# Kernel tuning notes

Hardware: AMD Instinct MI355X
Metric: run time of the kernel (lower is better)

Reference implementation:

```python
import jax, jax.numpy as jnp
import numpy as np

N = 50000          # nodes per side (variables == clauses here)
IN, HID, OUT = 64, 128, 128
H = 4              # attention heads (self and cross)
P = 2              # num_meta_paths
E = 640000         # edges per graph
NEG = 0.2          # leaky_relu negative slope


def _glorot(key, shape):
    fan = shape[-2] + shape[-1]
    return (jax.random.normal(key, shape) * jnp.sqrt(2.0 / fan)).astype(jnp.float32)


def _ln(x, g, b):
    mu = x.mean(-1, keepdims=True)
    v = ((x - mu) ** 2).mean(-1, keepdims=True)
    return (x - mu) / jnp.sqrt(v + 1e-5) * g + b


def _segment_softmax(s, seg, num):
    # s: [E, H]; softmax over edges sharing the same seg id
    smax = jax.ops.segment_max(s, seg, num_segments=num)
    e = jnp.exp(s - smax[seg])
    den = jax.ops.segment_sum(e, seg, num_segments=num)
    return e / (den[seg] + 1e-16)


def _agg(alpha, feats, src, dst, num):
    # out[d, h, c] = sum_{e: dst[e]=d} alpha[e,h] * feats[src[e], c]
    gathered = feats[src]  # [E, C]
    outs = [jax.ops.segment_sum(alpha[:, h:h + 1] * gathered, dst, num_segments=num)
            for h in range(alpha.shape[1])]
    return jnp.stack(outs, axis=1)  # [num, H, C]


def _hga_self(x, adj, W, att_l, att_r, bias):
    # homogeneous HGAConv with self loops, concat=False (mean over heads)
    n = x.shape[0]
    xl = x @ W.T                      # [N, C]
    al = xl @ att_l                   # [N, H]
    ar = xl @ att_r                   # [N, H]
    loops = jnp.arange(n)
    src = jnp.concatenate([adj[0], loops])
    dst = jnp.concatenate([adj[1], loops])
    score = al[dst] + ar[src]         # edge_score: a_l[adj[1]] + a_r[adj[0]]
    alpha = _segment_softmax(jax.nn.leaky_relu(score, NEG), dst, n)
    out = _agg(alpha, xl, src, dst, n).mean(axis=1)  # [N, C]
    return out + bias


def _hga_cross(xv, xc, adj, Wl, Wr, att_l, att_r, bias):
    # bipartite HGAConv: adj[1] indexes var nodes, adj[0] indexes cls nodes
    n, m = xv.shape[0], xc.shape[0]
    xl = xv @ Wl.T
    xr = xc @ Wr.T
    al = xl @ att_l
    ar = xr @ att_r
    ar_ = xl @ att_r
    al_ = xr @ att_l
    c_idx, v_idx = adj[0], adj[1]
    score = al[v_idx] + ar[c_idx]        # -> normalized per var node
    score_ = ar_[v_idx] + al_[c_idx]     # transposed direction -> per cls node
    alpha = _segment_softmax(jax.nn.leaky_relu(score, NEG), v_idx, n)
    alpha_ = _segment_softmax(jax.nn.leaky_relu(score_, NEG), c_idx, m)
    out_var = _agg(alpha, xr, c_idx, v_idx, n).mean(axis=1) + bias   # [n, OUT]
    out_cls = _agg(alpha_, xl, v_idx, c_idx, m).mean(axis=1) + bias  # [m, OUT]
    return out_var, out_cls


def setup_inputs() -> dict:
    key = jax.random.key(0)
    ks = jax.random.split(key, 32)
    d = {}
    d['x_var'] = jax.random.normal(ks[0], (N, IN), dtype=jnp.float32)
    d['x_cls'] = jax.random.normal(ks[1], (N, IN), dtype=jnp.float32)
    d['mp_var'] = jax.random.randint(ks[2], (P, 2, E), 0, N)
    d['mp_cls'] = jax.random.randint(ks[3], (P, 2, E), 0, N)
    d['adj_pos'] = jax.random.randint(ks[4], (2, E), 0, N)
    d['adj_neg'] = jax.random.randint(ks[5], (2, E), 0, N)
    d['W_var_emb'] = _glorot(ks[6], (HID, IN))
    d['W_cls_emb'] = _glorot(ks[7], (HID, IN))
    d['ln_var_g'] = jnp.ones(HID); d['ln_var_b'] = jnp.zeros(HID)
    d['ln_cls_g'] = jnp.ones(HID); d['ln_cls_b'] = jnp.zeros(HID)
    d['var_pw'] = jnp.ones(P); d['cls_pw'] = jnp.ones(P)
    d['sv_W'] = _glorot(ks[8], (P, HID, HID))
    d['sv_al'] = _glorot(ks[9], (P, HID, H))
    d['sv_ar'] = _glorot(ks[10], (P, HID, H))
    d['sv_b'] = jnp.zeros((P, HID))
    d['sc_W'] = _glorot(ks[11], (P, HID, HID))
    d['sc_al'] = _glorot(ks[12], (P, HID, H))
    d['sc_ar'] = _glorot(ks[13], (P, HID, H))
    d['sc_b'] = jnp.zeros((P, HID))
    d['cp_Wl'] = _glorot(ks[14], (OUT, HID))
    d['cp_Wr'] = _glorot(ks[15], (OUT, HID))
    d['cp_al'] = _glorot(ks[16], (OUT, H))
    d['cp_ar'] = _glorot(ks[17], (OUT, H))
    d['cp_b'] = jnp.zeros(OUT)
    d['cn_Wl'] = _glorot(ks[18], (OUT, HID))
    d['cn_Wr'] = _glorot(ks[19], (OUT, HID))
    d['cn_al'] = _glorot(ks[20], (OUT, H))
    d['cn_ar'] = _glorot(ks[21], (OUT, H))
    d['cn_b'] = jnp.zeros(OUT)
    return d


def reference(x_var, x_cls, mp_var, mp_cls, adj_pos, adj_neg,
              W_var_emb, W_cls_emb, ln_var_g, ln_var_b, ln_cls_g, ln_cls_b,
              var_pw, cls_pw, sv_W, sv_al, sv_ar, sv_b, sc_W, sc_al, sc_ar, sc_b,
              cp_Wl, cp_Wr, cp_al, cp_ar, cp_b, cn_Wl, cn_Wr, cn_al, cn_ar, cn_b):
    xv = x_var @ W_var_emb.T          # [N, HID]
    xc = x_cls @ W_cls_emb.T
    # pre-norm residual self-attention, weighted sum over meta paths
    hv = _ln(xv, ln_var_g, ln_var_b)
    hc = _ln(xc, ln_cls_g, ln_cls_b)
    av = sum(var_pw[p] * _hga_self(hv, mp_var[p], sv_W[p], sv_al[p], sv_ar[p], sv_b[p]) for p in range(P))
    ac = sum(cls_pw[p] * _hga_self(hc, mp_cls[p], sc_W[p], sc_al[p], sc_ar[p], sc_b[p]) for p in range(P))
    xv = xv + av
    xc = xc + ac
    # bipartite cross attention over positive / negative literal edges
    vpos, cpos = _hga_cross(xv, xc, adj_pos, cp_Wl, cp_Wr, cp_al, cp_ar, cp_b)
    vneg, cneg = _hga_cross(xv, xc, adj_neg, cn_Wl, cn_Wr, cn_al, cn_ar, cn_b)
    return jnp.stack([vpos + vneg, cpos + cneg])  # [2, N, OUT]
```

## Files before the change

### kernel.cpp

```cpp
#include <hip/hip_runtime.h>
#include <hip/hip_bf16.h>

#define NN 50000
#define EE 640000
#define NEG 0.2f
#define CAP 128

#define BSH 9
#define NBKT 98
#define FCAP 7168
#define CHUNKA 8192
#define PA_B 79

struct Ptr8 { const int* p[8]; };
struct MArgs { const float* w[8]; const float* al[8]; const float* ar[8]; };

struct SegArg {
    const int* starts;
    const int* counts;
    const unsigned short* srt;
    const float* adst;
    const float* asrc;
    const unsigned short* feats;
    const float* pw;
    int pwi;
    int hasLoop;
};

typedef __attribute__((ext_vector_type(8))) short short8;
typedef __attribute__((ext_vector_type(8))) unsigned short ushort8;
typedef __attribute__((ext_vector_type(4))) float floatx4;

__device__ __forceinline__ unsigned short f2bf(float x) {
    unsigned b = __float_as_uint(x);
    b = b + 0x7fffu + ((b >> 16) & 1u);
    return (unsigned short)(b >> 16);
}

__global__ void transpose_emb(const float* __restrict__ wev, const float* __restrict__ wec,
                              float* __restrict__ out)
{
    int i = blockIdx.x * 256 + threadIdx.x;
    if (i < 8192) { out[i] = wev[(i & 127) * 64 + (i >> 7)]; return; }
    if (i < 16384) { int j = i - 8192; out[i] = wec[(j & 127) * 64 + (j >> 7)]; }
}

__global__ void make_M(MArgs a, float* __restrict__ Mbuf)
{
    int b = blockIdx.x;
    const float* W  = a.w[b];
    const float* AL = a.al[b];
    const float* AR = a.ar[b];
    for (int e = threadIdx.x; e < 1024; e += 256) {
        int k = e >> 3, h = e & 7;
        const float* att = (h < 4) ? AL : AR;
        int hh = h & 3;
        float s = 0.f;
        for (int c = 0; c < 128; c++) s += W[c * 128 + k] * att[c * 4 + hh];
        Mbuf[b * 1024 + e] = s;
    }
}

__global__ void embed_ln(const float* __restrict__ x, const float* __restrict__ Wt,
                         const float* __restrict__ g, const float* __restrict__ b,
                         const float* __restrict__ pw, const float* __restrict__ sb,
                         float* __restrict__ F, float* __restrict__ C)
{
    __shared__ float lx[8][64];
    __shared__ float red[2][8][2];
    int c = threadIdx.x;
    int n0 = blockIdx.x * 8;
    for (int t = c; t < 8 * 64; t += 128) {
        lx[t >> 6][t & 63] = x[(size_t)(n0 + (t >> 6)) * 64 + (t & 63)];
    }
    __syncthreads();
    float acc[8];
#pragma unroll
    for (int m = 0; m < 8; m++) acc[m] = 0.f;
    for (int k = 0; k < 64; k++) {
        float w = Wt[k * 128 + c];
#pragma unroll
        for (int m = 0; m < 8; m++) acc[m] += lx[m][k] * w;
    }
    int lane = c & 63, wv = c >> 6;
#pragma unroll
    for (int m = 0; m < 8; m++) {
        float s1 = acc[m], s2 = acc[m] * acc[m];
        for (int off = 32; off; off >>= 1) { s1 += __shfl_xor(s1, off); s2 += __shfl_xor(s2, off); }
        if (lane == 0) { red[wv][m][0] = s1; red[wv][m][1] = s2; }
    }
    __syncthreads();
    float biassum = pw[0] * sb[c] + pw[1] * sb[128 + c];
    float gg = g[c], bb = b[c];
#pragma unroll
    for (int m = 0; m < 8; m++) {
        float s1 = red[0][m][0] + red[1][m][0];
        float s2 = red[0][m][1] + red[1][m][1];
        float mu  = s1 * (1.f / 128.f);
        float var = s2 * (1.f / 128.f) - mu * mu;
        float inv = rsqrtf(var + 1e-5f);
        float v = acc[m];
        size_t idx = (size_t)(n0 + m) * 128 + c;
        F[idx] = v + biassum;
        C[idx] = (v - mu) * inv * gg + bb;
    }
}

__global__ __launch_bounds__(256) void mfma_proj(
    const float* __restrict__ in,
    const float* __restrict__ W,
    const float* __restrict__ M,
    unsigned short* __restrict__ out_bf,
    float4* __restrict__ dl4, float4* __restrict__ dr4)
{
    __shared__ unsigned short WL[16384];
    __shared__ float ML[1024];

    int t = threadIdx.x;
    for (int i = t; i < 2048; i += 256) {
        int n = i >> 4, c16 = i & 15;
        const float* src = W + n * 128 + c16 * 8;
        short8 v;
#pragma unroll
        for (int j = 0; j < 8; j++) v[j] = (short)f2bf(src[j]);
        *(short8*)&WL[(n * 16 + (c16 ^ (n & 15))) * 8] = v;
    }
    for (int i = t; i < 1024; i += 256) ML[i] = M[i];
    __syncthreads();

    int w = t >> 6, lane = t & 63;
    int ln = lane & 15, quad = lane >> 4;
    int rbase = blockIdx.x * 64 + w * 16;
    int row = rbase + ln;
    int arow = (row < NN) ? row : (NN - 1);

    short8 afrag[4];
    float p[8];
#pragma unroll
    for (int h = 0; h < 8; h++) p[h] = 0.f;
#pragma unroll
    for (int kc = 0; kc < 4; kc++) {
        int k0 = kc * 32 + quad * 8;
        const float* ap = in + (size_t)arow * 128 + k0;
        float av[8];
#pragma unroll
        for (int j = 0; j < 8; j++) av[j] = ap[j];
#pragma unroll
        for (int j = 0; j < 8; j++) {
            afrag[kc][j] = (short)f2bf(av[j]);
            const float* mrow = &ML[(k0 + j) * 8];
#pragma unroll
            for (int h = 0; h < 8; h++) p[h] += av[j] * mrow[h];
        }
    }
#pragma unroll
    for (int h = 0; h < 8; h++) {
        p[h] += __shfl_xor(p[h], 16);
        p[h] += __shfl_xor(p[h], 32);
    }
    if (quad == 0 && row < NN) {
        dl4[row] = make_float4(p[0], p[1], p[2], p[3]);
        dr4[row] = make_float4(p[4], p[5], p[6], p[7]);
    }

#pragma unroll
    for (int ct = 0; ct < 8; ct++) {
        floatx4 acc = {0.f, 0.f, 0.f, 0.f};
#pragma unroll
        for (int kc = 0; kc < 4; kc++) {
            int c16 = kc * 4 + quad;
            int n = ct * 16 + ln;
            short8 bfr = *(const short8*)&WL[(n * 16 + (c16 ^ ln)) * 8];
            acc = __builtin_amdgcn_mfma_f32_16x16x32_bf16(afrag[kc], bfr, acc, 0, 0, 0);
        }
#pragma unroll
        for (int r = 0; r < 4; r++) {
            int rr = rbase + quad * 4 + r;
            if (rr < NN) out_bf[(size_t)rr * 128 + ct * 16 + ln] = f2bf(acc[r]);
        }
    }
}

__global__ void zero_bcnt(int* __restrict__ p)
{
    int i = blockIdx.x * 256 + threadIdx.x;
    if (i < 8 * NBKT) p[i] = 0;
}

__global__ void bucket_count(Ptr8 dst, int* __restrict__ bcnt)
{
    __shared__ int h[NBKT];
    int l = blockIdx.x / PA_B, cb = blockIdx.x % PA_B;
    const int* dp = dst.p[l];
    for (int i = threadIdx.x; i < NBKT; i += 256) h[i] = 0;
    __syncthreads();
    int e0 = cb * CHUNKA;
    for (int i = threadIdx.x; i < CHUNKA; i += 256) {
        int e = e0 + i;
        if (e < EE) atomicAdd(&h[dp[e] >> BSH], 1);
    }
    __syncthreads();
    for (int i = threadIdx.x; i < NBKT; i += 256)
        if (h[i]) atomicAdd(&bcnt[l * NBKT + i], h[i]);
}

__global__ void bucket_scan(const int* __restrict__ bcnt, int* __restrict__ bstart,
                            int* __restrict__ bcur)
{
    __shared__ int sh[NBKT];
    int l = blockIdx.x;
    for (int i = threadIdx.x; i < NBKT; i += 256) sh[i] = bcnt[l * NBKT + i];
    __syncthreads();
    if (threadIdx.x == 0) {
        int acc = 0;
        for (int i = 0; i < NBKT; i++) { int t = sh[i]; sh[i] = acc; acc += t; }
    }
    __syncthreads();
    for (int i = threadIdx.x; i < NBKT; i += 256) {
        bstart[l * (NBKT + 1) + i] = sh[i];
        bcur[l * NBKT + i] = sh[i];
    }
    if (threadIdx.x == 0) bstart[l * (NBKT + 1) + NBKT] = EE;
}

__global__ void bucket_place(Ptr8 src, Ptr8 dst, int* __restrict__ bcur,
                             unsigned* __restrict__ recs)
{
    __shared__ int h[NBKT];
    __shared__ int base[NBKT];
    int l = blockIdx.x / PA_B, cb = blockIdx.x % PA_B;
    const int* sp = src.p[l];
    const int* dp = dst.p[l];
    for (int i = threadIdx.x; i < NBKT; i += 256) h[i] = 0;
    __syncthreads();
    int e0 = cb * CHUNKA;
    for (int i = threadIdx.x; i < CHUNKA; i += 256) {
        int e = e0 + i;
        if (e < EE) atomicAdd(&h[dp[e] >> BSH], 1);
    }
    __syncthreads();
    for (int i = threadIdx.x; i < NBKT; i += 256) {
        int c = h[i];
        base[i] = c ? atomicAdd(&bcur[l * NBKT + i], c) : 0;
        h[i] = 0;
    }
    __syncthreads();
    unsigned* rl = recs + (size_t)l * EE;
    for (int i = threadIdx.x; i < CHUNKA; i += 256) {
        int e = e0 + i;
        if (e >= EE) continue;
        int d = dp[e];
        int b = d >> BSH;
        int pos = base[b] + atomicAdd(&h[b], 1);
        rl[pos] = ((unsigned)sp[e] << 16) | (unsigned)d;
    }
}

__global__ __launch_bounds__(256) void bucket_final(
    const unsigned* __restrict__ recs, const int* __restrict__ bstart,
    int* __restrict__ starts8, int* __restrict__ counts8,
    unsigned short* __restrict__ sortedU)
{
    __shared__ unsigned R[FCAP];
    __shared__ int cnt[512];
    __shared__ int cur[512];
    __shared__ int psum[256];
    int l = blockIdx.x / NBKT, b = blockIdx.x % NBKT;
    int d0 = b << BSH;
    int nd = min(512, NN - d0);
    int ebase = bstart[l * (NBKT + 1) + b];
    int ecnt  = bstart[l * (NBKT + 1) + b + 1] - ebase;
    const unsigned* rp = recs + (size_t)l * EE + ebase;
    int t = threadIdx.x;
    bool inLds = (ecnt <= FCAP);

    for (int i = t; i < 512; i += 256) cnt[i] = 0;
    __syncthreads();
    for (int i = t; i < ecnt; i += 256) {
        unsigned r = rp[i];
        if (inLds) R[i] = r;
        atomicAdd(&cnt[(r & 0xffffu) - d0], 1);
    }
    __syncthreads();
    int s0 = cnt[2 * t] + cnt[2 * t + 1];
    psum[t] = s0;
    __syncthreads();
    for (int off = 1; off < 256; off <<= 1) {
        int x = (t >= off) ? psum[t - off] : 0;
        __syncthreads();
        psum[t] += x;
        __syncthreads();
    }
    int excl = psum[t] - s0;
    cur[2 * t] = excl;
    cur[2 * t + 1] = excl + cnt[2 * t];
    __syncthreads();
    for (int i = t; i < nd; i += 256) {
        starts8[l * NN + d0 + i] = ebase + cur[i];
        counts8[l * NN + d0 + i] = cnt[i];
    }
    __syncthreads();
    unsigned short* so = sortedU + (size_t)l * EE + ebase;
    for (int i = t; i < ecnt; i += 256) {
        unsigned r = inLds ? R[i] : rp[i];
        int dloc = (int)(r & 0xffffu) - d0;
        int pos = atomicAdd(&cur[dloc], 1);
        so[pos] = (unsigned short)(r >> 16);
    }
}

__global__ __launch_bounds__(256) void agg_fused(
    SegArg A, SegArg B,
    const float* __restrict__ bias0, const float* __restrict__ bias1,
    float* __restrict__ acc, int mode)
{
    __shared__ float4 exSh[4][CAP];
    __shared__ int    sSh[4][CAP + 4];
    __shared__ float  wSh[4][CAP + 4];
    __shared__ float  cmb[4][128];

    int t = threadIdx.x;
    int slot = t >> 6;
    int w = slot & 1;
    int dh = slot >> 1;
    int lane = t & 63;
    int d = blockIdx.x * 2 + dh;

    const SegArg S = w ? B : A;

    int base = S.starts[d];
    int k = S.counts[d];
    int kTot = k + S.hasLoop;

    float4 ad = *(const float4*)(S.adst + (size_t)d * 4);
    float p0 = 0.f, p1 = 0.f, p2 = 0.f, p3 = 0.f;
    for (int i = lane; i < kTot; i += 64) {
        int s = (i < k) ? (int)S.srt[base + i] : d;
        float4 as = *(const float4*)(S.asrc + (size_t)s * 4);
        float v0 = ad.x + as.x, v1 = ad.y + as.y, v2 = ad.z + as.z, v3 = ad.w + as.w;
        v0 = v0 > 0.f ? v0 : NEG * v0;
        v1 = v1 > 0.f ? v1 : NEG * v1;
        v2 = v2 > 0.f ? v2 : NEG * v2;
        v3 = v3 > 0.f ? v3 : NEG * v3;
        float e0 = __expf(v0), e1 = __expf(v1), e2 = __expf(v2), e3 = __expf(v3);
        if (i < CAP) { exSh[slot][i] = make_float4(e0, e1, e2, e3); sSh[slot][i] = s; }
        p0 += e0; p1 += e1; p2 += e2; p3 += e3;
    }
#pragma unroll
    for (int off = 32; off; off >>= 1) {
        p0 += __shfl_xor(p0, off); p1 += __shfl_xor(p1, off);
        p2 += __shfl_xor(p2, off); p3 += __shfl_xor(p3, off);
    }
    float scale = 0.25f * (S.pw ? S.pw[S.pwi] : 1.0f);
    float den0 = p0 + 1e-16f, den1 = p1 + 1e-16f;
    float den2 = p2 + 1e-16f, den3 = p3 + 1e-16f;

    int kW = kTot < CAP ? kTot : CAP;
    for (int i = lane; i < kW; i += 64) {
        float4 ex = exSh[slot][i];
        wSh[slot][i] = scale * (ex.x / den0 + ex.y / den1 + ex.z / den2 + ex.w / den3);
    }
    if (kTot <= CAP) {
        int nPad = (kTot + 3) & ~3;
        for (int i = kTot + lane; i < nPad; i += 64) { wSh[slot][i] = 0.f; sSh[slot][i] = 0; }
    }
    __syncthreads();

    if (kTot <= CAP) {
        int g = lane >> 4, c8 = lane & 15;
        float a[8];
#pragma unroll
        for (int i = 0; i < 8; i++) a[i] = 0.f;
        int nIter = (kTot + 3) >> 2;
        for (int it = 0; it < nIter; ++it) {
            int j = it * 4 + g;
            float wgt = wSh[slot][j];
            int s = sSh[slot][j];
            ushort8 v = *(const ushort8*)(S.feats + (size_t)s * 128 + c8 * 8);
#pragma unroll
            for (int i = 0; i < 8; i++)
                a[i] += wgt * __uint_as_float((unsigned)(unsigned short)v[i] << 16);
        }
#pragma unroll
        for (int i = 0; i < 8; i++) {
            a[i] += __shfl_xor(a[i], 16);
            a[i] += __shfl_xor(a[i], 32);
        }
        if (lane < 16) {
#pragma unroll
            for (int i = 0; i < 8; i++) cmb[slot][lane * 8 + i] = a[i];
        }
    } else {
        float a0 = 0.f, a1 = 0.f;
        for (int j = 0; j < kTot; ++j) {
            float wgt; int s;
            if (j < CAP) { wgt = wSh[slot][j]; s = sSh[slot][j]; }
            else {
                s = (j < k) ? (int)S.srt[base + j] : d;
                float4 as = *(const float4*)(S.asrc + (size_t)s * 4);
                float v0 = ad.x + as.x, v1 = ad.y + as.y, v2 = ad.z + as.z, v3 = ad.w + as.w;
                v0 = v0 > 0.f ? v0 : NEG * v0;
                v1 = v1 > 0.f ? v1 : NEG * v1;
                v2 = v2 > 0.f ? v2 : NEG * v2;
                v3 = v3 > 0.f ? v3 : NEG * v3;
                wgt = scale * (__expf(v0) / den0 + __expf(v1) / den1 +
                               __expf(v2) / den2 + __expf(v3) / den3);
            }
            unsigned v = *(const unsigned*)(S.feats + (size_t)s * 128 + 2 * lane);
            a0 += wgt * __uint_as_float(v << 16);
            a1 += wgt * __uint_as_float(v & 0xffff0000u);
        }
        cmb[slot][2 * lane] = a0;
        cmb[slot][2 * lane + 1] = a1;
    }
    __syncthreads();

    {
        int dh2 = t >> 7;
        int c = t & 127;
        int dd = blockIdx.x * 2 + dh2;
        float sum = cmb[dh2 * 2][c] + cmb[dh2 * 2 + 1][c];
        size_t idx = (size_t)dd * 128 + c;
        if (mode) acc[idx] = bias0[c] + bias1[c] + sum;
        else      acc[idx] += sum;
    }
}

extern "C" void kernel_launch(void* const* d_in, const int* in_sizes, int n_in,
                              void* d_out, int out_size, void* d_ws, size_t ws_size,
                              hipStream_t stream)
{
    const float* x_var   = (const float*)d_in[0];
    const float* x_cls   = (const float*)d_in[1];
    const int*   mp_var  = (const int*)d_in[2];
    const int*   mp_cls  = (const int*)d_in[3];
    const int*   adj_pos = (const int*)d_in[4];
    const int*   adj_neg = (const int*)d_in[5];
    const float* W_var_emb = (const float*)d_in[6];
    const float* W_cls_emb = (const float*)d_in[7];
    const float* ln_var_g = (const float*)d_in[8];
    const float* ln_var_b = (const float*)d_in[9];
    const float* ln_cls_g = (const float*)d_in[10];
    const float* ln_cls_b = (const float*)d_in[11];
    const float* var_pw = (const float*)d_in[12];
    const float* cls_pw = (const float*)d_in[13];
    const float* sv_W  = (const float*)d_in[14];
    const float* sv_al = (const float*)d_in[15];
    const float* sv_ar = (const float*)d_in[16];
    const float* sv_b  = (const float*)d_in[17];
    const float* sc_W  = (const float*)d_in[18];
    const float* sc_al = (const float*)d_in[19];
    const float* sc_ar = (const float*)d_in[20];
    const float* sc_b  = (const float*)d_in[21];
    const float* cp_Wl = (const float*)d_in[22];
    const float* cp_Wr = (const float*)d_in[23];
    const float* cp_al = (const float*)d_in[24];
    const float* cp_ar = (const float*)d_in[25];
    const float* cp_b  = (const float*)d_in[26];
    const float* cn_Wl = (const float*)d_in[27];
    const float* cn_Wr = (const float*)d_in[28];
    const float* cn_al = (const float*)d_in[29];
    const float* cn_ar = (const float*)d_in[30];
    const float* cn_b  = (const float*)d_in[31];

    float* out0 = (float*)d_out;
    float* out1 = out0 + (size_t)NN * 128;

    float* ws = (float*)d_ws;
    size_t off = 0;
    auto alloc = [&](size_t n) { float* p = ws + off; off += n; return p; };
    float* Wt   = alloc(16384);
    float* Mbuf = alloc(8 * 1024);
    float* F   = alloc((size_t)NN * 128);
    float* G   = alloc((size_t)NN * 128);
    float* C   = alloc((size_t)NN * 128);
    float* D   = alloc((size_t)NN * 128);
    unsigned short* B1 = (unsigned short*)alloc((size_t)NN * 64);
    unsigned short* B2 = (unsigned short*)alloc((size_t)NN * 64);
    float* dl   = alloc(NN * 4);
    float* dr   = alloc(NN * 4);
    float* dl2  = alloc(NN * 4);
    float* dr2  = alloc(NN * 4);
    float* dl3  = alloc(NN * 4);
    float* dr3  = alloc(NN * 4);
    float* dl4  = alloc(NN * 4);
    float* dr4  = alloc(NN * 4);
    int* counts8 = (int*)alloc(8 * NN);
    int* starts8 = (int*)alloc(8 * NN);
    int* bcnt    = (int*)alloc(8 * NBKT);
    int* bstart  = (int*)alloc(8 * (NBKT + 1));
    int* bcur    = (int*)alloc(8 * NBKT);
    unsigned* recs = (unsigned*)alloc((size_t)8 * EE);
    unsigned short* sortedU = (unsigned short*)alloc((size_t)4 * EE);

    unsigned short* Pc = (unsigned short*)C;
    unsigned short* Pd = (unsigned short*)C + (size_t)NN * 128;

    const float* WtEv = Wt;
    const float* WtEc = Wt + 8192;

    Ptr8 srcP, dstP;
    srcP.p[0] = mp_var;            dstP.p[0] = mp_var + EE;
    srcP.p[1] = mp_var + 2 * EE;   dstP.p[1] = mp_var + 3 * EE;
    srcP.p[2] = mp_cls;            dstP.p[2] = mp_cls + EE;
    srcP.p[3] = mp_cls + 2 * EE;   dstP.p[3] = mp_cls + 3 * EE;
    srcP.p[4] = adj_pos;           dstP.p[4] = adj_pos + EE;
    srcP.p[5] = adj_pos + EE;      dstP.p[5] = adj_pos;
    srcP.p[6] = adj_neg;           dstP.p[6] = adj_neg + EE;
    srcP.p[7] = adj_neg + EE;      dstP.p[7] = adj_neg;

    MArgs ma;
    ma.w[0] = sv_W;           ma.al[0] = sv_al;        ma.ar[0] = sv_ar;
    ma.w[1] = sv_W + 16384;   ma.al[1] = sv_al + 512;  ma.ar[1] = sv_ar + 512;
    ma.w[2] = sc_W;           ma.al[2] = sc_al;        ma.ar[2] = sc_ar;
    ma.w[3] = sc_W + 16384;   ma.al[3] = sc_al + 512;  ma.ar[3] = sc_ar + 512;
    ma.w[4] = cp_Wl;          ma.al[4] = cp_al;        ma.ar[4] = cp_ar;
    ma.w[5] = cp_Wr;          ma.al[5] = cp_al;        ma.ar[5] = cp_ar;
    ma.w[6] = cn_Wl;          ma.al[6] = cn_al;        ma.ar[6] = cn_ar;
    ma.w[7] = cn_Wr;          ma.al[7] = cn_al;        ma.ar[7] = cn_ar;

    zero_bcnt<<<(8 * NBKT + 255) / 256, 256, 0, stream>>>(bcnt);
    bucket_count<<<8 * PA_B, 256, 0, stream>>>(dstP, bcnt);
    bucket_scan<<<8, 256, 0, stream>>>(bcnt, bstart, bcur);
    bucket_place<<<8 * PA_B, 256, 0, stream>>>(srcP, dstP, bcur, recs);
    bucket_final<<<8 * NBKT, 256, 0, stream>>>(recs, bstart, starts8, counts8, sortedU);

    transpose_emb<<<64, 256, 0, stream>>>(W_var_emb, W_cls_emb, Wt);
    make_M<<<8, 256, 0, stream>>>(ma, Mbuf);
    embed_ln<<<NN / 8, 128, 0, stream>>>(x_var, WtEv, ln_var_g, ln_var_b, var_pw, sv_b, F, C);
    embed_ln<<<NN / 8, 128, 0, stream>>>(x_cls, WtEc, ln_cls_g, ln_cls_b, cls_pw, sc_b, G, D);

    const int PB = (NN + 63) / 64;

    for (int side = 0; side < 2; ++side) {
        const float* h   = side ? D : C;
        float*       accp = side ? G : F;
        const float* pw  = side ? cls_pw : var_pw;
        int s0 = side * 2, s1 = side * 2 + 1;
        mfma_proj<<<PB, 256, 0, stream>>>(h, ma.w[s0], Mbuf + s0 * 1024,
                                          B1, (float4*)dl, (float4*)dr);
        mfma_proj<<<PB, 256, 0, stream>>>(h, ma.w[s1], Mbuf + s1 * 1024,
                                          B2, (float4*)dl2, (float4*)dr2);
        SegArg SA, SB;
        SA.starts = starts8 + s0 * NN; SA.counts = counts8 + s0 * NN;
        SA.srt = sortedU + (size_t)s0 * EE;
        SA.adst = dl;  SA.asrc = dr;  SA.feats = B1; SA.pw = pw; SA.pwi = 0; SA.hasLoop = 1;
        SB.starts = starts8 + s1 * NN; SB.counts = counts8 + s1 * NN;
        SB.srt = sortedU + (size_t)s1 * EE;
        SB.adst = dl2; SB.asrc = dr2; SB.feats = B2; SB.pw = pw; SB.pwi = 1; SB.hasLoop = 1;
        agg_fused<<<NN / 2, 256, 0, stream>>>(SA, SB, cp_b, cn_b, accp, 0);
    }

    mfma_proj<<<PB, 256, 0, stream>>>(F, ma.w[4], Mbuf + 4 * 1024,
                                      B1, (float4*)dl, (float4*)dr);
    mfma_proj<<<PB, 256, 0, stream>>>(G, ma.w[5], Mbuf + 5 * 1024,
                                      B2, (float4*)dl2, (float4*)dr2);
    mfma_proj<<<PB, 256, 0, stream>>>(F, ma.w[6], Mbuf + 6 * 1024,
                                      Pc, (float4*)dl3, (float4*)dr3);
    mfma_proj<<<PB, 256, 0, stream>>>(G, ma.w[7], Mbuf + 7 * 1024,
                                      Pd, (float4*)dl4, (float4*)dr4);

    {
        SegArg SA, SB;
        SA.starts = starts8 + 4 * NN; SA.counts = counts8 + 4 * NN;
        SA.srt = sortedU + (size_t)4 * EE;
        SA.adst = dl;  SA.asrc = dr2; SA.feats = B2; SA.pw = nullptr; SA.pwi = 0; SA.hasLoop = 0;
        SB.starts = starts8 + 6 * NN; SB.counts = counts8 + 6 * NN;
        SB.srt = sortedU + (size_t)6 * EE;
        SB.adst = dl3; SB.asrc = dr4; SB.feats = Pd; SB.pw = nullptr; SB.pwi = 0; SB.hasLoop = 0;
        agg_fused<<<NN / 2, 256, 0, stream>>>(SA, SB, cp_b, cn_b, out0, 1);
    }
    {
        SegArg SA, SB;
        SA.starts = starts8 + 5 * NN; SA.counts = counts8 + 5 * NN;
        SA.srt = sortedU + (size_t)5 * EE;
        SA.adst = dl2; SA.asrc = dr;  SA.feats = B1; SA.pw = nullptr; SA.pwi = 0; SA.hasLoop = 0;
        SB.starts = starts8 + 7 * NN; SB.counts = counts8 + 7 * NN;
        SB.srt = sortedU + (size_t)7 * EE;
        SB.adst = dl4; SB.asrc = dr3; SB.feats = Pc; SB.pw = nullptr; SB.pwi = 0; SB.hasLoop = 0;
        agg_fused<<<NN / 2, 256, 0, stream>>>(SA, SB, cp_b, cn_b, out1, 1);
    }
}
```

Measured before the change: 772.4 us.

## Fuse paired projections sharing an input, unroll gather by two, precompute reciprocals

Pairs of projection launches that read the same input matrix are merged into one kernel. It loads the A fragments once, computes both score sets, and restages the second weight matrix in shared memory between the two MFMA passes. That removes one full read of the input and several launches. Separately, the aggregation loop now processes two gathered neighbour rows per iteration to expose more memory-level parallelism, with padding widened to multiples of eight. Per-edge divisions are replaced by multiplications with precomputed scaled reciprocals. The cost is higher register use in the fused projection and a serialised W restage inside each block.

Result: faster. 754.4 us (-2.3%).

```diff
diff --git a/kernel.cpp b/kernel.cpp
--- a/kernel.cpp
+++ b/kernel.cpp
@@ -106,17 +106,9 @@
     }
 }
 
-__global__ __launch_bounds__(256) void mfma_proj(
-    const float* __restrict__ in,
-    const float* __restrict__ W,
-    const float* __restrict__ M,
-    unsigned short* __restrict__ out_bf,
-    float4* __restrict__ dl4, float4* __restrict__ dr4)
-{
-    __shared__ unsigned short WL[16384];
-    __shared__ float ML[1024];
-
-    int t = threadIdx.x;
+__device__ __forceinline__ void stage_W(const float* __restrict__ W,
+                                        unsigned short* __restrict__ WL, int t)
+{
     for (int i = t; i < 2048; i += 256) {
         int n = i >> 4, c16 = i & 15;
         const float* src = W + n * 128 + c16 * 8;
@@ -125,7 +117,22 @@
         for (int j = 0; j < 8; j++) v[j] = (short)f2bf(src[j]);
         *(short8*)&WL[(n * 16 + (c16 ^ (n & 15))) * 8] = v;
     }
-    for (int i = t; i < 1024; i += 256) ML[i] = M[i];
+}
+
+__global__ __launch_bounds__(256) void mfma_proj2(
+    const float* __restrict__ in,
+    const float* __restrict__ W0, const float* __restrict__ W1,
+    const float* __restrict__ M0, const float* __restrict__ M1,
+    unsigned short* __restrict__ ob0, unsigned short* __restrict__ ob1,
+    float4* __restrict__ dl0, float4* __restrict__ dr0,
+    float4* __restrict__ dl1, float4* __restrict__ dr1)
+{
+    __shared__ unsigned short WL[16384];
+    __shared__ float ML[2048];
+
+    int t = threadIdx.x;
+    stage_W(W0, WL, t);
+    for (int i = t; i < 1024; i += 256) { ML[i] = M0[i]; ML[1024 + i] = M1[i]; }
     __syncthreads();
 
     int w = t >> 6, lane = t & 63;
@@ -135,9 +142,9 @@
     int arow = (row < NN) ? row : (NN - 1);
 
     short8 afrag[4];
-    float p[8];
-#pragma unroll
-    for (int h = 0; h < 8; h++) p[h] = 0.f;
+    float p[16];
+#pragma unroll
+    for (int h = 0; h < 16; h++) p[h] = 0.f;
 #pragma unroll
     for (int kc = 0; kc < 4; kc++) {
         int k0 = kc * 32 + quad * 8;
@@ -148,19 +155,22 @@
 #pragma unroll
         for (int j = 0; j < 8; j++) {
             afrag[kc][j] = (short)f2bf(av[j]);
-            const float* mrow = &ML[(k0 + j) * 8];
-#pragma unroll
-            for (int h = 0; h < 8; h++) p[h] += av[j] * mrow[h];
-        }
-    }
-#pragma unroll
-    for (int h = 0; h < 8; h++) {
+            const float* m0 = &ML[(k0 + j) * 8];
+            const float* m1 = &ML[1024 + (k0 + j) * 8];
+#pragma unroll
+            for (int h = 0; h < 8; h++) { p[h] += av[j] * m0[h]; p[8 + h] += av[j] * m1[h]; }
+        }
+    }
+#pragma unroll
+    for (int h = 0; h < 16; h++) {
         p[h] += __shfl_xor(p[h], 16);
         p[h] += __shfl_xor(p[h], 32);
     }
     if (quad == 0 && row < NN) {
-        dl4[row] = make_float4(p[0], p[1], p[2], p[3]);
-        dr4[row] = make_float4(p[4], p[5], p[6], p[7]);
+        dl0[row] = make_float4(p[0], p[1], p[2], p[3]);
+        dr0[row] = make_float4(p[4], p[5], p[6], p[7]);
+        dl1[row] = make_float4(p[8], p[9], p[10], p[11]);
+        dr1[row] = make_float4(p[12], p[13], p[14], p[15]);
     }
 
 #pragma unroll
@@ -176,7 +186,26 @@
 #pragma unroll
         for (int r = 0; r < 4; r++) {
             int rr = rbase + quad * 4 + r;
-            if (rr < NN) out_bf[(size_t)rr * 128 + ct * 16 + ln] = f2bf(acc[r]);
+            if (rr < NN) ob0[(size_t)rr * 128 + ct * 16 + ln] = f2bf(acc[r]);
+        }
+    }
+    __syncthreads();
+    stage_W(W1, WL, t);
+    __syncthreads();
+#pragma unroll
+    for (int ct = 0; ct < 8; ct++) {
+        floatx4 acc = {0.f, 0.f, 0.f, 0.f};
+#pragma unroll
+        for (int kc = 0; kc < 4; kc++) {
+            int c16 = kc * 4 + quad;
+            int n = ct * 16 + ln;
+            short8 bfr = *(const short8*)&WL[(n * 16 + (c16 ^ ln)) * 8];
+            acc = __builtin_amdgcn_mfma_f32_16x16x32_bf16(afrag[kc], bfr, acc, 0, 0, 0);
+        }
+#pragma unroll
+        for (int r = 0; r < 4; r++) {
+            int rr = rbase + quad * 4 + r;
+            if (rr < NN) ob1[(size_t)rr * 128 + ct * 16 + ln] = f2bf(acc[r]);
         }
     }
 }
@@ -315,8 +344,8 @@
     float* __restrict__ acc, int mode)
 {
     __shared__ float4 exSh[4][CAP];
-    __shared__ int    sSh[4][CAP + 4];
-    __shared__ float  wSh[4][CAP + 4];
+    __shared__ int    sSh[4][CAP + 8];
+    __shared__ float  wSh[4][CAP + 8];
     __shared__ float  cmb[4][128];
 
     int t = threadIdx.x;
@@ -352,16 +381,18 @@
         p2 += __shfl_xor(p2, off); p3 += __shfl_xor(p3, off);
     }
     float scale = 0.25f * (S.pw ? S.pw[S.pwi] : 1.0f);
-    float den0 = p0 + 1e-16f, den1 = p1 + 1e-16f;
-    float den2 = p2 + 1e-16f, den3 = p3 + 1e-16f;
+    float i0 = scale / (p0 + 1e-16f);
+    float i1 = scale / (p1 + 1e-16f);
+    float i2 = scale / (p2 + 1e-16f);
+    float i3 = scale / (p3 + 1e-16f);
 
     int kW = kTot < CAP ? kTot : CAP;
     for (int i = lane; i < kW; i += 64) {
         float4 ex = exSh[slot][i];
-        wSh[slot][i] = scale * (ex.x / den0 + ex.y / den1 + ex.z / den2 + ex.w / den3);
+        wSh[slot][i] = ex.x * i0 + ex.y * i1 + ex.z * i2 + ex.w * i3;
     }
     if (kTot <= CAP) {
-        int nPad = (kTot + 3) & ~3;
+        int nPad = (kTot + 7) & ~7;
         for (int i = kTot + lane; i < nPad; i += 64) { wSh[slot][i] = 0.f; sSh[slot][i] = 0; }
     }
     __syncthreads();
@@ -371,15 +402,19 @@
         float a[8];
 #pragma unroll
         for (int i = 0; i < 8; i++) a[i] = 0.f;
-        int nIter = (kTot + 3) >> 2;
+        int nIter = (kTot + 7) >> 3;
         for (int it = 0; it < nIter; ++it) {
-            int j = it * 4 + g;
-            float wgt = wSh[slot][j];
-            int s = sSh[slot][j];
-            ushort8 v = *(const ushort8*)(S.feats + (size_t)s * 128 + c8 * 8);
-#pragma unroll
-            for (int i = 0; i < 8; i++)
-                a[i] += wgt * __uint_as_float((unsigned)(unsigned short)v[i] << 16);
+            int j0 = it * 8 + g;
+            int j1 = j0 + 4;
+            float w0 = wSh[slot][j0], w1 = wSh[slot][j1];
+            int s0 = sSh[slot][j0], s1 = sSh[slot][j1];
+            ushort8 v0 = *(const ushort8*)(S.feats + (size_t)s0 * 128 + c8 * 8);
+            ushort8 v1 = *(const ushort8*)(S.feats + (size_t)s1 * 128 + c8 * 8);
+#pragma unroll
+            for (int i = 0; i < 8; i++) {
+                a[i] += w0 * __uint_as_float((unsigned)(unsigned short)v0[i] << 16);
+                a[i] += w1 * __uint_as_float((unsigned)(unsigned short)v1[i] << 16);
+            }
         }
 #pragma unroll
         for (int i = 0; i < 8; i++) {
@@ -403,8 +438,7 @@
                 v1 = v1 > 0.f ? v1 : NEG * v1;
                 v2 = v2 > 0.f ? v2 : NEG * v2;
                 v3 = v3 > 0.f ? v3 : NEG * v3;
-                wgt = scale * (__expf(v0) / den0 + __expf(v1) / den1 +
-                               __expf(v2) / den2 + __expf(v3) / den3);
+                wgt = __expf(v0) * i0 + __expf(v1) * i1 + __expf(v2) * i2 + __expf(v3) * i3;
             }
             unsigned v = *(const unsigned*)(S.feats + (size_t)s * 128 + 2 * lane);
             a0 += wgt * __uint_as_float(v << 16);
@@ -533,14 +567,15 @@
     const int PB = (NN + 63) / 64;
 
     for (int side = 0; side < 2; ++side) {
-        const float* h   = side ? D : C;
+        const float* h    = side ? D : C;
         float*       accp = side ? G : F;
-        const float* pw  = side ? cls_pw : var_pw;
+        const float* pw   = side ? cls_pw : var_pw;
         int s0 = side * 2, s1 = side * 2 + 1;
-        mfma_proj<<<PB, 256, 0, stream>>>(h, ma.w[s0], Mbuf + s0 * 1024,
-                                          B1, (float4*)dl, (float4*)dr);
-        mfma_proj<<<PB, 256, 0, stream>>>(h, ma.w[s1], Mbuf + s1 * 1024,
-                                          B2, (float4*)dl2, (float4*)dr2);
+        mfma_proj2<<<PB, 256, 0, stream>>>(h, ma.w[s0], ma.w[s1],
+                                           Mbuf + s0 * 1024, Mbuf + s1 * 1024,
+                                           B1, B2,
+                                           (float4*)dl, (float4*)dr,
+                                           (float4*)dl2, (float4*)dr2);
         SegArg SA, SB;
         SA.starts = starts8 + s0 * NN; SA.counts = counts8 + s0 * NN;
         SA.srt = sortedU + (size_t)s0 * EE;
@@ -551,14 +586,16 @@
         agg_fused<<<NN / 2, 256, 0, stream>>>(SA, SB, cp_b, cn_b, accp, 0);
     }
 
-    mfma_proj<<<PB, 256, 0, stream>>>(F, ma.w[4], Mbuf + 4 * 1024,
-                                      B1, (float4*)dl, (float4*)dr);
-    mfma_proj<<<PB, 256, 0, stream>>>(G, ma.w[5], Mbuf + 5 * 1024,
-                                      B2, (float4*)dl2, (float4*)dr2);
-    mfma_proj<<<PB, 256, 0, stream>>>(F, ma.w[6], Mbuf + 6 * 1024,
-                                      Pc, (float4*)dl3, (float4*)dr3);
-    mfma_proj<<<PB, 256, 0, stream>>>(G, ma.w[7], Mbuf + 7 * 1024,
-                                      Pd, (float4*)dl4, (float4*)dr4);
+    mfma_proj2<<<PB, 256, 0, stream>>>(F, ma.w[4], ma.w[6],
+                                       Mbuf + 4 * 1024, Mbuf + 6 * 1024,
+                                       B1, Pc,
+                                       (float4*)dl, (float4*)dr,
+                                       (float4*)dl3, (float4*)dr3);
+    mfma_proj2<<<PB, 256, 0, stream>>>(G, ma.w[5], ma.w[7],
+                                       Mbuf + 5 * 1024, Mbuf + 7 * 1024,
+                                       B2, Pd,
+                                       (float4*)dl2, (float4*)dr2,
+                                       (float4*)dl4, (float4*)dr4);
 
     {
         SegArg SA, SB;
```
